# Optimization experiments

Hardware: AMD Instinct MI355X
Metric: run time of the kernel (lower is better)

## Reference

```python
import jax, jax.numpy as jnp
import numpy as np

B, N, D, E = 4, 2048, 1024, 4
H = 4 * D  # expert hidden (mult=4)


def setup_inputs() -> dict:
    key = jax.random.key(0)
    ks = jax.random.split(key, 8)
    std = 0.02
    return {
        "x": jax.random.normal(ks[0], (B, N, D), jnp.float32),
        "W_slot": jax.random.normal(ks[1], (E * D, D), jnp.float32) * std,
        "u_slot": jax.random.normal(ks[2], (D,), jnp.float32),
        "sigma_slot": jnp.ones((1,), jnp.float32),
        "W1": jax.random.normal(ks[3], (E, H, D), jnp.float32) * std,
        "b1": jnp.zeros((E, H), jnp.float32),
        "u1": jax.random.normal(ks[4], (E, D), jnp.float32),
        "sig1": jnp.ones((E,), jnp.float32),
        "W2": jax.random.normal(ks[5], (E, D, H), jnp.float32) * std,
        "b2": jnp.zeros((E, D), jnp.float32),
        "u2": jax.random.normal(ks[6], (E, H), jnp.float32),
        "sig2": jnp.ones((E,), jnp.float32),
    }


def _sn_weight(W, u, sigma):
    # One power-iteration step (no_grad in torch -> stop_gradient), then
    # sigma_spec = v^T W u'; weight = W / sigma_spec * learnable sigma.
    v = W @ u
    v = jax.lax.stop_gradient(v / jnp.linalg.norm(v))
    u2 = W.T @ v
    u2 = jax.lax.stop_gradient(u2 / jnp.linalg.norm(u2))
    s = jnp.einsum('c,cd,d->', v, W, u2)
    return W * (sigma / s)


def reference(x, W_slot, u_slot, sigma_slot, W1, b1, u1, sig1, W2, b2, u2, sig2):
    b, n, d = x.shape
    e = W1.shape[0]
    s = n // e  # slots per expert; n divisible by e -> no padding, no mask

    # dynamic slot embeddings from consecutive-segment means
    Wsl = _sn_weight(W_slot, u_slot, sigma_slot[0])          # [e*d, d]
    xm = x.reshape(b, s, e, d).mean(axis=2)                   # [b, s, d]
    slot_embeds = (xm @ Wsl.T).reshape(b, s, e, d)
    slot_embeds = slot_embeds.transpose(0, 2, 1, 3)           # [b, e, s, d]

    logits = jnp.einsum('bnd,besd->bnes', x, slot_embeds)     # [b, n, e, s]
    dispatch = jax.nn.softmax(logits, axis=1)                 # softmax over n
    combine = jax.nn.softmax(logits.reshape(b, n, e * s), axis=-1)

    slots = jnp.einsum('bnd,bnes->ebsd', x, dispatch)         # [e, b, s, d]

    # per-expert FFN with spectral-normed weights (vectorized over experts)
    W1n = jax.vmap(_sn_weight)(W1, u1, sig1)                  # [e, H, d]
    W2n = jax.vmap(_sn_weight)(W2, u2, sig2)                  # [e, d, H]
    h = jax.nn.gelu(jnp.einsum('ebsd,ehd->ebsh', slots, W1n) + b1[:, None, None, :],
                    approximate=False)
    y = jnp.einsum('ebsh,edh->ebsd', h, W2n) + b2[:, None, None, :]

    out = y.transpose(1, 0, 2, 3).reshape(b, e * s, d)        # [b, e*s, d]
    return jnp.einsum('bsd,bns->bnd', out, combine)           # [b, n, d]
```

## Files before the change

kernel.cpp:

```cpp
#include <hip/hip_runtime.h>
#include <hip/hip_bf16.h>
#include <math.h>

constexpr int CB  = 4;
constexpr int CN  = 2048;
constexpr int CD  = 1024;
constexpr int CE  = 4;
constexpr int CS  = 512;
constexpr int CH  = 4096;
constexpr int CES = 2048;

typedef unsigned short u16;
typedef unsigned int   u32;
typedef __bf16 bf16x8 __attribute__((ext_vector_type(8)));
typedef float  f32x4  __attribute__((ext_vector_type(4)));

__device__ __forceinline__ u16 f2bf(float x) {
  u32 u = __float_as_uint(x);
  u = (u + 0x7FFF + ((u >> 16) & 1)) >> 16;
  return (u16)u;
}

__device__ __forceinline__ void gl2lds16(const void* g, void* l) {
  __builtin_amdgcn_global_load_lds(
      (const __attribute__((address_space(1))) void*)g,
      (__attribute__((address_space(3))) void*)l, 16, 0, 0);
}

__device__ __forceinline__ void xcd_swz(int& bx, int& by, int& bz) {
  u32 gx = gridDim.x, gy = gridDim.y;
  u32 w = blockIdx.x + gx * (blockIdx.y + gy * blockIdx.z);
  u32 nwg = gx * gy * gridDim.z;
  u32 q = nwg >> 3;
  u32 wg = (w & 7) * q + (w >> 3);
  bx = wg % gx;
  u32 r = wg / gx;
  by = r % gy;
  bz = r / gy;
}


__global__ __launch_bounds__(256) void gemv_rows_k(const float* __restrict__ W,
    const float* __restrict__ u, float* __restrict__ t1, int M, int K, int ustride) {
  int bi = blockIdx.y;
  int row = blockIdx.x * 4 + (threadIdx.x >> 6);
  int lane = threadIdx.x & 63;
  const float* Wr = W + ((long)bi * M + row) * K;
  const float* ub = u + (long)bi * ustride;
  float s = 0.f;
  for (int k = lane; k < K; k += 64) s += Wr[k] * ub[k];
#pragma unroll
  for (int off = 32; off; off >>= 1) s += __shfl_down(s, off, 64);
  if (lane == 0) t1[bi * M + row] = s;
}

__global__ __launch_bounds__(256) void gemv_cols_k(const float* __restrict__ W,
    const float* __restrict__ t1, float* __restrict__ t2,
    u16* __restrict__ bh, u16* __restrict__ bl, int M, int K) {
  int bi = blockIdx.z;
  int k = blockIdx.x * 256 + threadIdx.x;
  int m0 = blockIdx.y * 256;
  const float* Wb = W + (long)bi * M * K;
  const float* tb = t1 + bi * M;
  u16* bhb = bh + (long)bi * M * K;
  u16* blb = bl ? bl + (long)bi * M * K : nullptr;
  float s = 0.f;
#pragma unroll 4
  for (int m = 0; m < 256; m++) {
    long idx = (long)(m0 + m) * K + k;
    float w = Wb[idx];
    s += w * tb[m0 + m];
    u16 h = f2bf(w);
    bhb[idx] = h;
    if (blb) blb[idx] = f2bf(w - __uint_as_float((u32)h << 16));
  }
  atomicAdd(&t2[bi * K + k], s);
}

__global__ __launch_bounds__(256) void scale_k(const float* __restrict__ t1,
    const float* __restrict__ t2, const float* __restrict__ sig,
    float* __restrict__ out, int M, int K) {
  int bi = blockIdx.x;
  int tid = threadIdx.x;
  __shared__ float red[256];
  float s1 = 0.f;
  for (int i = tid; i < M; i += 256) { float v = t1[bi * M + i]; s1 += v * v; }
  red[tid] = s1; __syncthreads();
  for (int w = 128; w; w >>= 1) { if (tid < w) red[tid] += red[tid + w]; __syncthreads(); }
  float n1 = red[0]; __syncthreads();
  float s2 = 0.f;
  for (int i = tid; i < K; i += 256) { float v = t2[bi * K + i]; s2 += v * v; }
  red[tid] = s2; __syncthreads();
  for (int w = 128; w; w >>= 1) { if (tid < w) red[tid] += red[tid + w]; __syncthreads(); }
  if (tid == 0) out[bi] = sig[bi] * sqrtf(n1 / red[0]);
}

__global__ __launch_bounds__(256) void xm_split_k(const float* __restrict__ x,
    u16* __restrict__ hi, u16* __restrict__ lo) {
  int idx = blockIdx.x * 256 + threadIdx.x;
  int d  = idx & (CD - 1);
  int si = (idx >> 10) & (CS - 1);
  int b  = idx >> 19;
  const float* xp = x + ((long)(b * CN + si * 4)) * CD + d;
  float v = 0.25f * (xp[0] + xp[CD] + xp[2 * CD] + xp[3 * CD]);
  u16 h = f2bf(v);
  hi[idx] = h;
  lo[idx] = f2bf(v - __uint_as_float((u32)h << 16));
}

__global__ __launch_bounds__(256) void split_k(const float* __restrict__ in,
    u16* __restrict__ hi, u16* __restrict__ lo) {
  long i = ((long)blockIdx.x * 256 + threadIdx.x) * 8;
  float4 a = *(const float4*)(in + i);
  float4 b = *(const float4*)(in + i + 4);
  float v[8] = {a.x, a.y, a.z, a.w, b.x, b.y, b.z, b.w};
  u16 oh[8], ol[8];
#pragma unroll
  for (int c = 0; c < 8; c++) {
    u16 h = f2bf(v[c]);
    oh[c] = h;
    ol[c] = f2bf(v[c] - __uint_as_float((u32)h << 16));
  }
  *(uint4*)(hi + i) = *(const uint4*)oh;
  *(uint4*)(lo + i) = *(const uint4*)ol;
}

__global__ __launch_bounds__(256) void colstat_part_k(const float* __restrict__ lg,
    float* __restrict__ pmax, float* __restrict__ psum) {
  int es = blockIdx.x * 256 + threadIdx.x;
  int sl = blockIdx.y;
  int b  = blockIdx.z;
  const float* p = lg + ((long)(b * CN + sl * 256)) * CES + es;
  float m = -1e30f, s = 0.f;
  for (int i = 0; i < 256; i++) {
    float v = p[(long)i * CES];
    if (v > m) { s *= __expf(m - v); m = v; }
    s += __expf(v - m);
  }
  int o = (b * 8 + sl) * CES + es;
  pmax[o] = m; psum[o] = s;
}

__global__ __launch_bounds__(256) void colstat_comb_k(const float* __restrict__ pmax,
    const float* __restrict__ psum, float* __restrict__ cmax, float* __restrict__ csum) {
  int idx = blockIdx.x * 256 + threadIdx.x;
  int b = idx >> 11;
  int es = idx & (CES - 1);
  float m = -1e30f;
#pragma unroll
  for (int sl = 0; sl < 8; sl++) m = fmaxf(m, pmax[(b * 8 + sl) * CES + es]);
  float s = 0.f;
#pragma unroll
  for (int sl = 0; sl < 8; sl++)
    s += psum[(b * 8 + sl) * CES + es] * __expf(pmax[(b * 8 + sl) * CES + es] - m);
  cmax[idx] = m; csum[idx] = s;
}

__global__ __launch_bounds__(256) void rowcomb_k(const float* __restrict__ lg,
                                                 u16* __restrict__ outB) {
  __shared__ float red[8];
  long row = blockIdx.x;
  const float* p = lg + row * CES + threadIdx.x * 8;
  float4 a = *(const float4*)p;
  float4 b = *(const float4*)(p + 4);
  float v[8] = {a.x, a.y, a.z, a.w, b.x, b.y, b.z, b.w};
  float m = v[0];
#pragma unroll
  for (int c = 1; c < 8; c++) m = fmaxf(m, v[c]);
#pragma unroll
  for (int off = 32; off; off >>= 1) m = fmaxf(m, __shfl_xor(m, off, 64));
  int wv = threadIdx.x >> 6;
  if ((threadIdx.x & 63) == 0) red[wv] = m;
  __syncthreads();
  m = fmaxf(fmaxf(red[0], red[1]), fmaxf(red[2], red[3]));
  float s = 0.f;
#pragma unroll
  for (int c = 0; c < 8; c++) { v[c] = __expf(v[c] - m); s += v[c]; }
#pragma unroll
  for (int off = 32; off; off >>= 1) s += __shfl_xor(s, off, 64);
  if ((threadIdx.x & 63) == 0) red[4 + wv] = s;
  __syncthreads();
  float inv = 1.f / (red[4] + red[5] + red[6] + red[7]);
  u16 o[8];
#pragma unroll
  for (int c = 0; c < 8; c++) o[c] = f2bf(v[c] * inv);
  *(uint4*)(outB + row * CES + threadIdx.x * 8) = *(const uint4*)o;
}

__global__ __launch_bounds__(256) void tr_f2b_k(const float* __restrict__ in,
    u16* __restrict__ out, const float* __restrict__ sub, int R, int C, int expmode) {
  __shared__ u16 t[32][33];
  int z = blockIdx.z;
  long ibase = (long)z * R * C;
  int r0 = blockIdx.y * 32, c0 = blockIdx.x * 32;
  int tx = threadIdx.x & 31, ty = threadIdx.x >> 5;
  float cm = expmode ? sub[(long)z * C + c0 + tx] : 0.f;
  for (int rr = ty; rr < 32; rr += 8) {
    float v = in[ibase + (long)(r0 + rr) * C + c0 + tx];
    if (expmode) v = __expf(v - cm);
    t[tx][rr] = f2bf(v);
  }
  __syncthreads();
  for (int cc = ty; cc < 32; cc += 8)
    out[ibase + (long)(c0 + cc) * R + r0 + tx] = t[cc][tx];
}

__global__ __launch_bounds__(256) void tr_b2b_k(const u16* __restrict__ in,
                                                u16* __restrict__ out, int R, int C) {
  __shared__ u16 t[32][33];
  int z = blockIdx.z;
  long ibase = (long)z * R * C;
  int r0 = blockIdx.y * 32, c0 = blockIdx.x * 32;
  int tx = threadIdx.x & 31, ty = threadIdx.x >> 5;
  for (int rr = ty; rr < 32; rr += 8)
    t[tx][rr] = in[ibase + (long)(r0 + rr) * C + c0 + tx];
  __syncthreads();
  for (int cc = ty; cc < 32; cc += 8)
    out[ibase + (long)(c0 + cc) * R + r0 + tx] = t[cc][tx];
}

struct MEpSESplit {
  u16* hi; u16* lo; const float* scale;
  __device__ void store(int z, int m, int n, float v) const {
    v *= scale[0];
    int b = m >> 9, si = m & 511, ei = n >> 10, di = n & 1023;
    long o = ((long)(b * CES + ei * 512 + si)) * CD + di;
    u16 h = f2bf(v);
    hi[o] = h;
    lo[o] = f2bf(v - __uint_as_float((u32)h << 16));
  }
};
struct MEpLogits {
  float* lg;
  __device__ void store(int b, int m, int n, float v) const {
    lg[((long)(b * CN + m)) * CES + n] = v;
  }
};
struct MEpSlots {
  u16* sb; const float* __restrict__ csum;
  __device__ void store(int b, int m, int n, float v) const {
    float inv = 1.f / csum[b * CES + m];
    int e = m >> 9, si = m & 511;
    sb[((long)(e * 2048 + b * 512 + si)) * CD + n] = f2bf(v * inv);
  }
};
struct MEpGelu {
  u16* h; const float* __restrict__ scales; const float* __restrict__ b1;
  __device__ void store(int e, int m, int n, float v) const {
    float xg = v * scales[1 + e] + b1[e * CH + n];
    float g = 0.5f * xg * (1.f + erff(xg * 0.70710678118654752f));
    h[((long)(e * 2048 + m)) * CH + n] = f2bf(g);
  }
};
struct MEpY {
  u16* ob; const float* __restrict__ scales; const float* __restrict__ b2;
  __device__ void store(int e, int m, int n, float v) const {
    int b = m >> 9, si = m & 511;
    ob[((long)(b * CES + e * 512 + si)) * CD + n] = f2bf(v * scales[5 + e] + b2[e * CD + n]);
  }
};
struct MEpOut {
  float* o;
  __device__ void store(int b, int m, int n, float v) const {
    o[((long)(b * CN + m)) * CD + n] = v;
  }
};


template <class EP>
__global__ __launch_bounds__(256) void mgemm_k(const u16* __restrict__ A, long Azs, int ldA,
                                               const u16* __restrict__ B, long Bzs, int ldB,
                                               EP ep, int K) {
  constexpr int BK = 32;
  __shared__ __align__(16) u16 As[128 * BK];
  __shared__ __align__(16) u16 Bs[128 * BK];
  int bx, by, bz;
  xcd_swz(bx, by, bz);
  const int tid = threadIdx.x;
  const int wid = tid >> 6, lane = tid & 63;
  const int m0 = by * 128, n0 = bx * 128;
  const u16* Az = A + (long)bz * Azs;
  const u16* Bz = B + (long)bz * Bzs;
  const int wr = wid >> 1, wc = wid & 1;
  const int srow = lane >> 2;
  const int sk8  = (lane & 3) * 8;

  f32x4 acc[4][4];
  f32x4 zero = {0.f, 0.f, 0.f, 0.f};
#pragma unroll
  for (int i = 0; i < 4; i++)
#pragma unroll
    for (int j = 0; j < 4; j++) acc[i][j] = zero;

  for (int k0 = 0; k0 < K; k0 += BK) {
#pragma unroll
    for (int i = 0; i < 2; i++) {
      int chunk = i * 4 + wid;
      int r = chunk * 16 + srow;
      gl2lds16(Az + (long)(m0 + r) * ldA + k0 + sk8, (char*)As + chunk * 1024);
      gl2lds16(Bz + (long)(n0 + r) * ldB + k0 + sk8, (char*)Bs + chunk * 1024);
    }
    __syncthreads();
    bf16x8 af[4], bfr[4];
#pragma unroll
    for (int i = 0; i < 4; i++) {
      int arow = wr * 64 + i * 16 + (lane & 15);
      af[i] = *(const bf16x8*)&As[arow * BK + (lane >> 4) * 8];
      int brow = wc * 64 + i * 16 + (lane & 15);
      bfr[i] = *(const bf16x8*)&Bs[brow * BK + (lane >> 4) * 8];
    }
#pragma unroll
    for (int i = 0; i < 4; i++)
#pragma unroll
      for (int j = 0; j < 4; j++)
        acc[i][j] = __builtin_amdgcn_mfma_f32_16x16x32_bf16(af[i], bfr[j], acc[i][j], 0, 0, 0);
    __syncthreads();
  }
#pragma unroll
  for (int i = 0; i < 4; i++) {
    int grow = m0 + wr * 64 + i * 16 + (lane >> 4) * 4;
#pragma unroll
    for (int j = 0; j < 4; j++) {
      int gcol = n0 + wc * 64 + j * 16 + (lane & 15);
#pragma unroll
      for (int r = 0; r < 4; r++)
        ep.store(bz, grow + r, gcol, acc[i][j][r]);
    }
  }
}

template <class EP>
__global__ __launch_bounds__(256) void mgemm3_k(const u16* __restrict__ Ah,
                                                const u16* __restrict__ Al, long Azs, int ldA,
                                                const u16* __restrict__ Bh,
                                                const u16* __restrict__ Bl, long Bzs, int ldB,
                                                EP ep, int K) {
  constexpr int BK = 32;
  __shared__ __align__(16) u16 Ahs[128 * BK];
  __shared__ __align__(16) u16 Als[128 * BK];
  __shared__ __align__(16) u16 Bhs[128 * BK];
  __shared__ __align__(16) u16 Bls[128 * BK];
  int bx, by, bz;
  xcd_swz(bx, by, bz);
  const int tid = threadIdx.x;
  const int wid = tid >> 6, lane = tid & 63;
  const int m0 = by * 128, n0 = bx * 128;
  const u16* Ahz = Ah + (long)bz * Azs;
  const u16* Alz = Al + (long)bz * Azs;
  const u16* Bhz = Bh + (long)bz * Bzs;
  const u16* Blz = Bl + (long)bz * Bzs;
  const int wr = wid >> 1, wc = wid & 1;
  const int srow = lane >> 2;
  const int sk8  = (lane & 3) * 8;

  f32x4 acc[4][4];
  f32x4 zero = {0.f, 0.f, 0.f, 0.f};
#pragma unroll
  for (int i = 0; i < 4; i++)
#pragma unroll
    for (int j = 0; j < 4; j++) acc[i][j] = zero;

  for (int k0 = 0; k0 < K; k0 += BK) {
#pragma unroll
    for (int i = 0; i < 2; i++) {
      int chunk = i * 4 + wid;
      int r = chunk * 16 + srow;
      long ao = (long)(m0 + r) * ldA + k0 + sk8;
      long bo = (long)(n0 + r) * ldB + k0 + sk8;
      gl2lds16(Ahz + ao, (char*)Ahs + chunk * 1024);
      gl2lds16(Alz + ao, (char*)Als + chunk * 1024);
      gl2lds16(Bhz + bo, (char*)Bhs + chunk * 1024);
      gl2lds16(Blz + bo, (char*)Bls + chunk * 1024);
    }
    __syncthreads();
    bf16x8 ah[4], al[4], bh[4], bl[4];
#pragma unroll
    for (int i = 0; i < 4; i++) {
      int arow = wr * 64 + i * 16 + (lane & 15);
      int aoff = arow * BK + (lane >> 4) * 8;
      ah[i] = *(const bf16x8*)&Ahs[aoff];
      al[i] = *(const bf16x8*)&Als[aoff];
      int brow = wc * 64 + i * 16 + (lane & 15);
      int boff = brow * BK + (lane >> 4) * 8;
      bh[i] = *(const bf16x8*)&Bhs[boff];
      bl[i] = *(const bf16x8*)&Bls[boff];
    }
#pragma unroll
    for (int i = 0; i < 4; i++)
#pragma unroll
      for (int j = 0; j < 4; j++) {
        acc[i][j] = __builtin_amdgcn_mfma_f32_16x16x32_bf16(ah[i], bh[j], acc[i][j], 0, 0, 0);
        acc[i][j] = __builtin_amdgcn_mfma_f32_16x16x32_bf16(al[i], bh[j], acc[i][j], 0, 0, 0);
        acc[i][j] = __builtin_amdgcn_mfma_f32_16x16x32_bf16(ah[i], bl[j], acc[i][j], 0, 0, 0);
      }
    __syncthreads();
  }
#pragma unroll
  for (int i = 0; i < 4; i++) {
    int grow = m0 + wr * 64 + i * 16 + (lane >> 4) * 4;
#pragma unroll
    for (int j = 0; j < 4; j++) {
      int gcol = n0 + wc * 64 + j * 16 + (lane & 15);
#pragma unroll
      for (int r = 0; r < 4; r++)
        ep.store(bz, grow + r, gcol, acc[i][j][r]);
    }
  }
}

extern "C" void kernel_launch(void* const* d_in, const int* in_sizes, int n_in,
                              void* d_out, int out_size, void* d_ws, size_t ws_size,
                              hipStream_t stream) {
  const float* x          = (const float*)d_in[0];
  const float* W_slot     = (const float*)d_in[1];
  const float* u_slot     = (const float*)d_in[2];
  const float* sigma_slot = (const float*)d_in[3];
  const float* W1         = (const float*)d_in[4];
  const float* b1         = (const float*)d_in[5];
  const float* u1         = (const float*)d_in[6];
  const float* sig1       = (const float*)d_in[7];
  const float* W2         = (const float*)d_in[8];
  const float* b2         = (const float*)d_in[9];
  const float* u2         = (const float*)d_in[10];
  const float* sig2       = (const float*)d_in[11];
  float* out = (float*)d_out;

  char* ws = (char*)d_ws;
  size_t off = 0;
  auto alloc = [&](size_t bytes) -> char* {
    char* p = ws + off;
    off += (bytes + 255) & ~(size_t)255;
    return p;
  };
  float* t1s = (float*)alloc(4096 * 4);
  float* t1a = (float*)alloc(4 * 4096 * 4);
  float* t1b = (float*)alloc(4 * 1024 * 4);
  float* t2s = (float*)alloc(1024 * 4);
  float* t2a = (float*)alloc(4 * 1024 * 4);
  float* t2b = (float*)alloc(4 * 4096 * 4);
  float* scales = (float*)alloc(16 * 4);
  float* pmax   = (float*)alloc((size_t)CB * 8 * CES * 4);
  float* psum   = (float*)alloc((size_t)CB * 8 * CES * 4);
  float* cmax   = (float*)alloc((size_t)CB * CES * 4);
  float* csum   = (float*)alloc((size_t)CB * CES * 4);
  char* regAB   = alloc((size_t)CB * CN * CD * 2 * 2);
  char* regBB   = alloc((size_t)CB * CES * CD * 2 * 2);
  char* regL    = alloc((size_t)CB * CN * CES * 4);
  char* regS    = alloc((size_t)CE * CB * CS * CD * 2);
  u16* W1b      = (u16*)alloc((size_t)CE * CH * CD * 2);
  u16* W2b      = (u16*)alloc((size_t)CE * CD * CH * 2);

  u16*   xh      = (u16*)regAB;
  u16*   xl      = (u16*)(regAB + (size_t)CB * CN * CD * 2);
  u16*   dispT   = (u16*)regAB;
  u16*   combineB= (u16*)regAB;
  u16*   seh     = (u16*)regBB;
  u16*   sel     = (u16*)(regBB + (size_t)CB * CES * CD * 2);
  u16*   xT      = (u16*)regBB;
  u16*   outbufB = (u16*)(regBB + (size_t)CB * CES * CD * 2);
  float* logits  = (float*)regL;
  u16*   hbuf    = (u16*)regL;
  u16*   xmh     = (u16*)regL;
  u16*   xml     = (u16*)(regL + (size_t)CB * CS * CD * 2);
  u16*   wslh    = (u16*)(regL + (size_t)2 * CB * CS * CD * 2);
  u16*   wsll    = (u16*)(regL + (size_t)2 * CB * CS * CD * 2 + (size_t)CE * CD * CD * 2);
  u16*   slotsB  = (u16*)regS;
  u16*   outbufT = (u16*)regS;

  hipMemsetAsync(t2s, 0, 1024 * 4, stream);
  hipMemsetAsync(t2a, 0, 4 * 1024 * 4, stream);
  hipMemsetAsync(t2b, 0, 4 * 4096 * 4, stream);

  gemv_rows_k<<<dim3(4096 / 4, 1), 256, 0, stream>>>(W_slot, u_slot, t1s, 4096, 1024, 0);
  gemv_rows_k<<<dim3(4096 / 4, 4), 256, 0, stream>>>(W1, u1, t1a, CH, CD, CD);
  gemv_rows_k<<<dim3(1024 / 4, 4), 256, 0, stream>>>(W2, u2, t1b, CD, CH, CH);
  gemv_cols_k<<<dim3(1024 / 256, 4096 / 256, 1), 256, 0, stream>>>(W_slot, t1s, t2s, wslh, wsll, 4096, 1024);
  gemv_cols_k<<<dim3(1024 / 256, 4096 / 256, 4), 256, 0, stream>>>(W1, t1a, t2a, W1b, nullptr, CH, CD);
  gemv_cols_k<<<dim3(4096 / 256, 1024 / 256, 4), 256, 0, stream>>>(W2, t1b, t2b, W2b, nullptr, CD, CH);
  scale_k<<<1, 256, 0, stream>>>(t1s, t2s, sigma_slot, scales + 0, 4096, 1024);
  scale_k<<<4, 256, 0, stream>>>(t1a, t2a, sig1, scales + 1, CH, CD);
  scale_k<<<4, 256, 0, stream>>>(t1b, t2b, sig2, scales + 5, CD, CH);

  split_k<<<(int)((size_t)CB * CN * CD / 8 / 256), 256, 0, stream>>>(x, xh, xl);
  xm_split_k<<<(CB * CS * CD) / 256, 256, 0, stream>>>(x, xmh, xml);

  mgemm3_k<<<dim3(4096 / 128, 2048 / 128, 1), 256, 0, stream>>>(
      xmh, xml, 0L, CD, wslh, wsll, 0L, CD, MEpSESplit{seh, sel, scales}, CD);

  mgemm3_k<<<dim3(CES / 128, CN / 128, CB), 256, 0, stream>>>(
      xh, xl, (long)CN * CD, CD, seh, sel, (long)CES * CD, CD,
      MEpLogits{logits}, CD);

  colstat_part_k<<<dim3(CES / 256, 8, CB), 256, 0, stream>>>(logits, pmax, psum);
  colstat_comb_k<<<(CB * CES) / 256, 256, 0, stream>>>(pmax, psum, cmax, csum);

  tr_f2b_k<<<dim3(CES / 32, CN / 32, CB), 256, 0, stream>>>(logits, dispT, cmax, CN, CES, 1);
  tr_f2b_k<<<dim3(CD / 32, CN / 32, CB), 256, 0, stream>>>(x, xT, nullptr, CN, CD, 0);

  mgemm_k<<<dim3(CD / 128, CES / 128, CB), 256, 0, stream>>>(
      dispT, (long)CES * CN, CN, xT, (long)CD * CN, CN, MEpSlots{slotsB, csum}, CN);

  rowcomb_k<<<CB * CN, 256, 0, stream>>>(logits, combineB);

  mgemm_k<<<dim3(CH / 128, 2048 / 128, CE), 256, 0, stream>>>(
      slotsB, (long)2048 * CD, CD, W1b, (long)CH * CD, CD, MEpGelu{hbuf, scales, b1}, CD);

  mgemm_k<<<dim3(CD / 128, 2048 / 128, CE), 256, 0, stream>>>(
      hbuf, (long)2048 * CH, CH, W2b, (long)CD * CH, CH, MEpY{outbufB, scales, b2}, CH);

  tr_b2b_k<<<dim3(CD / 32, CES / 32, CB), 256, 0, stream>>>(outbufB, outbufT, CES, CD);

  mgemm_k<<<dim3(CD / 128, CN / 128, CB), 256, 0, stream>>>(
      combineB, (long)CN * CES, CES, outbufT, (long)CD * CES, CES, MEpOut{out}, CES);

  (void)in_sizes; (void)n_in; (void)out_size; (void)ws_size;
}
```

Baseline: 924.3 us.

## Fuse x splitting kernels, template GEMM tiles, and drop output transpose

```diff
diff --git a/kernel.cpp b/kernel.cpp
--- a/kernel.cpp
+++ b/kernel.cpp
@@ -95,34 +95,45 @@
   if (tid == 0) out[bi] = sig[bi] * sqrtf(n1 / red[0]);
 }
 
-__global__ __launch_bounds__(256) void xm_split_k(const float* __restrict__ x,
-    u16* __restrict__ hi, u16* __restrict__ lo) {
+__global__ __launch_bounds__(256) void xsplit_fused_k(const float* __restrict__ x,
+    u16* __restrict__ xh, u16* __restrict__ xl,
+    u16* __restrict__ xmh, u16* __restrict__ xml) {
   int idx = blockIdx.x * 256 + threadIdx.x;
-  int d  = idx & (CD - 1);
-  int si = (idx >> 10) & (CS - 1);
-  int b  = idx >> 19;
-  const float* xp = x + ((long)(b * CN + si * 4)) * CD + d;
-  float v = 0.25f * (xp[0] + xp[CD] + xp[2 * CD] + xp[3 * CD]);
-  u16 h = f2bf(v);
-  hi[idx] = h;
-  lo[idx] = f2bf(v - __uint_as_float((u32)h << 16));
-}
-
-__global__ __launch_bounds__(256) void split_k(const float* __restrict__ in,
-    u16* __restrict__ hi, u16* __restrict__ lo) {
-  long i = ((long)blockIdx.x * 256 + threadIdx.x) * 8;
-  float4 a = *(const float4*)(in + i);
-  float4 b = *(const float4*)(in + i + 4);
-  float v[8] = {a.x, a.y, a.z, a.w, b.x, b.y, b.z, b.w};
+  int d8 = idx & (CD / 8 - 1);
+  int si = (idx >> 7) & (CS - 1);
+  int b  = idx >> 16;
+  long rbase = ((long)(b * CN + si * 4)) * CD + d8 * 8;
+  float vr[4][8];
+#pragma unroll
+  for (int r = 0; r < 4; r++) {
+    float4 a = *(const float4*)(x + rbase + (long)r * CD);
+    float4 c = *(const float4*)(x + rbase + (long)r * CD + 4);
+    vr[r][0]=a.x; vr[r][1]=a.y; vr[r][2]=a.z; vr[r][3]=a.w;
+    vr[r][4]=c.x; vr[r][5]=c.y; vr[r][6]=c.z; vr[r][7]=c.w;
+  }
+#pragma unroll
+  for (int r = 0; r < 4; r++) {
+    u16 oh[8], ol[8];
+#pragma unroll
+    for (int c = 0; c < 8; c++) {
+      u16 h = f2bf(vr[r][c]);
+      oh[c] = h;
+      ol[c] = f2bf(vr[r][c] - __uint_as_float((u32)h << 16));
+    }
+    *(uint4*)(xh + rbase + (long)r * CD) = *(const uint4*)oh;
+    *(uint4*)(xl + rbase + (long)r * CD) = *(const uint4*)ol;
+  }
+  long mbase = ((long)(b * CS + si)) * CD + d8 * 8;
   u16 oh[8], ol[8];
 #pragma unroll
   for (int c = 0; c < 8; c++) {
-    u16 h = f2bf(v[c]);
+    float v = 0.25f * (vr[0][c] + vr[1][c] + vr[2][c] + vr[3][c]);
+    u16 h = f2bf(v);
     oh[c] = h;
-    ol[c] = f2bf(v[c] - __uint_as_float((u32)h << 16));
-  }
-  *(uint4*)(hi + i) = *(const uint4*)oh;
-  *(uint4*)(lo + i) = *(const uint4*)ol;
+    ol[c] = f2bf(v - __uint_as_float((u32)h << 16));
+  }
+  *(uint4*)(xmh + mbase) = *(const uint4*)oh;
+  *(uint4*)(xml + mbase) = *(const uint4*)ol;
 }
 
 __global__ __launch_bounds__(256) void colstat_part_k(const float* __restrict__ lg,
@@ -205,20 +216,6 @@
     out[ibase + (long)(c0 + cc) * R + r0 + tx] = t[cc][tx];
 }
 
-__global__ __launch_bounds__(256) void tr_b2b_k(const u16* __restrict__ in,
-                                                u16* __restrict__ out, int R, int C) {
-  __shared__ u16 t[32][33];
-  int z = blockIdx.z;
-  long ibase = (long)z * R * C;
-  int r0 = blockIdx.y * 32, c0 = blockIdx.x * 32;
-  int tx = threadIdx.x & 31, ty = threadIdx.x >> 5;
-  for (int rr = ty; rr < 32; rr += 8)
-    t[tx][rr] = in[ibase + (long)(r0 + rr) * C + c0 + tx];
-  __syncthreads();
-  for (int cc = ty; cc < 32; cc += 8)
-    out[ibase + (long)(c0 + cc) * R + r0 + tx] = t[cc][tx];
-}
-
 struct MEpSESplit {
   u16* hi; u16* lo; const float* scale;
   __device__ void store(int z, int m, int n, float v) const {
@@ -252,11 +249,11 @@
     h[((long)(e * 2048 + m)) * CH + n] = f2bf(g);
   }
 };
-struct MEpY {
-  u16* ob; const float* __restrict__ scales; const float* __restrict__ b2;
+struct MEpYT {
+  u16* ot; const float* __restrict__ scales; const float* __restrict__ b2;
   __device__ void store(int e, int m, int n, float v) const {
-    int b = m >> 9, si = m & 511;
-    ob[((long)(b * CES + e * 512 + si)) * CD + n] = f2bf(v * scales[5 + e] + b2[e * CD + n]);
+    int b = n >> 9, si = n & 511;
+    ot[((long)(b * CD + m)) * CES + e * 512 + si] = f2bf(v * scales[5 + e] + b2[e * CD + m]);
   }
 };
 struct MEpOut {
@@ -267,61 +264,73 @@
 };
 
 
-template <class EP>
+template <int BN, int BK, class EP>
 __global__ __launch_bounds__(256) void mgemm_k(const u16* __restrict__ A, long Azs, int ldA,
                                                const u16* __restrict__ B, long Bzs, int ldB,
                                                EP ep, int K) {
-  constexpr int BK = 32;
-  __shared__ __align__(16) u16 As[128 * BK];
-  __shared__ __align__(16) u16 Bs[128 * BK];
+  constexpr int BM = 128;
+  constexpr int FI = 4;
+  constexpr int FJ = BN / 32;
+  constexpr int RPL = 512 / BK;
+  constexpr int NGRP = (BM + BN) / RPL;
+  constexpr int GPW = NGRP / 4;
+  __shared__ __align__(16) u16 S[(BM + BN) * BK];
   int bx, by, bz;
   xcd_swz(bx, by, bz);
   const int tid = threadIdx.x;
   const int wid = tid >> 6, lane = tid & 63;
-  const int m0 = by * 128, n0 = bx * 128;
+  const int m0 = by * BM, n0 = bx * BN;
   const u16* Az = A + (long)bz * Azs;
   const u16* Bz = B + (long)bz * Bzs;
   const int wr = wid >> 1, wc = wid & 1;
-  const int srow = lane >> 2;
-  const int sk8  = (lane & 3) * 8;
-
-  f32x4 acc[4][4];
+  const int lrow = lane / (BK / 8);
+  const int lk   = (lane % (BK / 8)) * 8;
+
+  f32x4 acc[FI][FJ];
   f32x4 zero = {0.f, 0.f, 0.f, 0.f};
 #pragma unroll
-  for (int i = 0; i < 4; i++)
-#pragma unroll
-    for (int j = 0; j < 4; j++) acc[i][j] = zero;
+  for (int i = 0; i < FI; i++)
+#pragma unroll
+    for (int j = 0; j < FJ; j++) acc[i][j] = zero;
 
   for (int k0 = 0; k0 < K; k0 += BK) {
 #pragma unroll
-    for (int i = 0; i < 2; i++) {
-      int chunk = i * 4 + wid;
-      int r = chunk * 16 + srow;
-      gl2lds16(Az + (long)(m0 + r) * ldA + k0 + sk8, (char*)As + chunk * 1024);
-      gl2lds16(Bz + (long)(n0 + r) * ldB + k0 + sk8, (char*)Bs + chunk * 1024);
+    for (int g = 0; g < GPW; g++) {
+      int grp = g * 4 + wid;
+      int row = grp * RPL + lrow;
+      const u16* src = (row < BM)
+          ? Az + (long)(m0 + row) * ldA + k0 + lk
+          : Bz + (long)(n0 + row - BM) * ldB + k0 + lk;
+      gl2lds16(src, (char*)S + grp * 1024);
     }
     __syncthreads();
-    bf16x8 af[4], bfr[4];
-#pragma unroll
-    for (int i = 0; i < 4; i++) {
-      int arow = wr * 64 + i * 16 + (lane & 15);
-      af[i] = *(const bf16x8*)&As[arow * BK + (lane >> 4) * 8];
-      int brow = wc * 64 + i * 16 + (lane & 15);
-      bfr[i] = *(const bf16x8*)&Bs[brow * BK + (lane >> 4) * 8];
-    }
-#pragma unroll
-    for (int i = 0; i < 4; i++)
-#pragma unroll
-      for (int j = 0; j < 4; j++)
-        acc[i][j] = __builtin_amdgcn_mfma_f32_16x16x32_bf16(af[i], bfr[j], acc[i][j], 0, 0, 0);
+#pragma unroll
+    for (int kk2 = 0; kk2 < BK / 32; kk2++) {
+      bf16x8 af[FI], bfr[FJ];
+#pragma unroll
+      for (int i = 0; i < FI; i++) {
+        int arow = wr * 64 + i * 16 + (lane & 15);
+        af[i] = *(const bf16x8*)&S[arow * BK + kk2 * 32 + (lane >> 4) * 8];
+      }
+#pragma unroll
+      for (int j = 0; j < FJ; j++) {
+        int brow = BM + wc * (BN / 2) + j * 16 + (lane & 15);
+        bfr[j] = *(const bf16x8*)&S[brow * BK + kk2 * 32 + (lane >> 4) * 8];
+      }
+#pragma unroll
+      for (int i = 0; i < FI; i++)
+#pragma unroll
+        for (int j = 0; j < FJ; j++)
+          acc[i][j] = __builtin_amdgcn_mfma_f32_16x16x32_bf16(af[i], bfr[j], acc[i][j], 0, 0, 0);
+    }
     __syncthreads();
   }
 #pragma unroll
-  for (int i = 0; i < 4; i++) {
+  for (int i = 0; i < FI; i++) {
     int grow = m0 + wr * 64 + i * 16 + (lane >> 4) * 4;
 #pragma unroll
-    for (int j = 0; j < 4; j++) {
-      int gcol = n0 + wc * 64 + j * 16 + (lane & 15);
+    for (int j = 0; j < FJ; j++) {
+      int gcol = n0 + wc * (BN / 2) + j * 16 + (lane & 15);
 #pragma unroll
       for (int r = 0; r < 4; r++)
         ep.store(bz, grow + r, gcol, acc[i][j][r]);
@@ -457,7 +466,6 @@
   u16*   seh     = (u16*)regBB;
   u16*   sel     = (u16*)(regBB + (size_t)CB * CES * CD * 2);
   u16*   xT      = (u16*)regBB;
-  u16*   outbufB = (u16*)(regBB + (size_t)CB * CES * CD * 2);
   float* logits  = (float*)regL;
   u16*   hbuf    = (u16*)regL;
   u16*   xmh     = (u16*)regL;
@@ -481,8 +489,7 @@
   scale_k<<<4, 256, 0, stream>>>(t1a, t2a, sig1, scales + 1, CH, CD);
   scale_k<<<4, 256, 0, stream>>>(t1b, t2b, sig2, scales + 5, CD, CH);
 
-  split_k<<<(int)((size_t)CB * CN * CD / 8 / 256), 256, 0, stream>>>(x, xh, xl);
-  xm_split_k<<<(CB * CS * CD) / 256, 256, 0, stream>>>(x, xmh, xml);
+  xsplit_fused_k<<<(CB * CS * (CD / 8)) / 256, 256, 0, stream>>>(x, xh, xl, xmh, xml);
 
   mgemm3_k<<<dim3(4096 / 128, 2048 / 128, 1), 256, 0, stream>>>(
       xmh, xml, 0L, CD, wslh, wsll, 0L, CD, MEpSESplit{seh, sel, scales}, CD);
@@ -497,20 +504,18 @@
   tr_f2b_k<<<dim3(CES / 32, CN / 32, CB), 256, 0, stream>>>(logits, dispT, cmax, CN, CES, 1);
   tr_f2b_k<<<dim3(CD / 32, CN / 32, CB), 256, 0, stream>>>(x, xT, nullptr, CN, CD, 0);
 
-  mgemm_k<<<dim3(CD / 128, CES / 128, CB), 256, 0, stream>>>(
+  mgemm_k<64, 64><<<dim3(CD / 64, CES / 128, CB), 256, 0, stream>>>(
       dispT, (long)CES * CN, CN, xT, (long)CD * CN, CN, MEpSlots{slotsB, csum}, CN);
 
   rowcomb_k<<<CB * CN, 256, 0, stream>>>(logits, combineB);
 
-  mgemm_k<<<dim3(CH / 128, 2048 / 128, CE), 256, 0, stream>>>(
+  mgemm_k<128, 32><<<dim3(CH / 128, 2048 / 128, CE), 256, 0, stream>>>(
       slotsB, (long)2048 * CD, CD, W1b, (long)CH * CD, CD, MEpGelu{hbuf, scales, b1}, CD);
 
-  mgemm_k<<<dim3(CD / 128, 2048 / 128, CE), 256, 0, stream>>>(
-      hbuf, (long)2048 * CH, CH, W2b, (long)CD * CH, CH, MEpY{outbufB, scales, b2}, CH);
-
-  tr_b2b_k<<<dim3(CD / 32, CES / 32, CB), 256, 0, stream>>>(outbufB, outbufT, CES, CD);
-
-  mgemm_k<<<dim3(CD / 128, CN / 128, CB), 256, 0, stream>>>(
+  mgemm_k<64, 64><<<dim3(2048 / 64, CD / 128, CE), 256, 0, stream>>>(
+      W2b, (long)CD * CH, CH, hbuf, (long)2048 * CH, CH, MEpYT{outbufT, scales, b2}, CH);
+
+  mgemm_k<64, 64><<<dim3(CD / 64, CN / 128, CB), 256, 0, stream>>>(
       combineB, (long)CN * CES, CES, outbufT, (long)CD * CES, CES, MEpOut{out}, CES);
 
   (void)in_sizes; (void)n_in; (void)out_size; (void)ws_size;
```

Result: faster. 897.3 us (-2.9%).
